# Kernel tuning notes

Hardware: AMD Instinct MI355X
Metric: run time of the kernel (lower is better)

## Reference

```python
import jax, jax.numpy as jnp
import numpy as np

B, T, D, H = 1024, 64, 256, 256  # batch, time steps, input_size, hidden_size


def setup_inputs() -> dict:
    key = jax.random.key(0)
    ks = jax.random.split(key, 5)
    s = 0.05
    return {
        "input_data": jax.random.normal(ks[0], (B, T, D), jnp.float32),
        # nn.Linear(2H+T, 1)
        "W_attn": jax.random.normal(ks[1], (1, 2 * H + T), jnp.float32) * s,
        "b_attn": jnp.zeros((1,), jnp.float32),
        # nn.LSTM(input_size=D, hidden_size=H, num_layers=1); gate order i,f,g,o
        "W_ih": jax.random.normal(ks[2], (4 * H, D), jnp.float32) * s,
        "W_hh": jax.random.normal(ks[3], (4 * H, H), jnp.float32) * s,
        "b_ih": jnp.zeros((4 * H,), jnp.float32),
        "b_hh": jnp.zeros((4 * H,), jnp.float32),
    }


def _encoder(input_data, W_attn, b_attn, W_ih, W_hh, b_ih, b_hh):
    Bv, Tv, Dv = input_data.shape
    Hv = W_hh.shape[1]
    # attn_linear applied to concat([h, c, x_series]) decomposes exactly into
    # three dot products (same math, no giant concat materialized each step).
    w_h = W_attn[0, :Hv]            # (H,)  weight on hidden part
    w_c = W_attn[0, Hv:2 * Hv]      # (H,)  weight on cell part
    w_x = W_attn[0, 2 * Hv:]        # (T,)  weight on per-feature time series
    # input_data.permute(0,2,1) @ w_x is constant across steps -> precompute.
    x_score = jnp.einsum('btd,t->bd', input_data, w_x) + b_attn[0]  # (B, D)

    xs = jnp.moveaxis(input_data, 1, 0)  # (T, B, D)

    def step(carry, x_t):
        h, c = carry                              # each (B, H)
        s_hc = h @ w_h + c @ w_c                  # (B,) same across features
        attn = jax.nn.softmax(s_hc[:, None] + x_score, axis=1)  # (B, D)
        w_in = attn * x_t                         # weighted input, (B, D)
        gates = w_in @ W_ih.T + h @ W_hh.T + b_ih + b_hh  # (B, 4H)
        i, f, g, o = jnp.split(gates, 4, axis=1)
        c_new = jax.nn.sigmoid(f) * c + jax.nn.sigmoid(i) * jnp.tanh(g)
        h_new = jax.nn.sigmoid(o) * jnp.tanh(c_new)
        return (h_new, c_new), (w_in, h_new)

    h0 = jnp.zeros((Bv, Hv), input_data.dtype)
    c0 = jnp.zeros((Bv, Hv), input_data.dtype)
    _, (ws, hs) = jax.lax.scan(step, (h0, c0), xs)
    input_weighted = jnp.moveaxis(ws, 0, 1)  # (B, T, D)
    input_encoded = jnp.moveaxis(hs, 0, 1)   # (B, T, H)
    return input_weighted, input_encoded


def reference(input_data, W_attn, b_attn, W_ih, W_hh, b_ih, b_hh):
    return _encoder(input_data, W_attn, b_attn, W_ih, W_hh, b_ih, b_hh)
```

## Files before the change

### kernel.cpp

```cpp
#include <hip/hip_runtime.h>
#include <hip/hip_bf16.h>
#include <stdint.h>

#define B_ 1024
#define T_ 64
#define D_ 256
#define H_ 256
#define G_ 1024

typedef float f32x4 __attribute__((ext_vector_type(4)));
typedef __bf16 bf16x8 __attribute__((ext_vector_type(8)));
typedef unsigned int u32x4 __attribute__((ext_vector_type(4)));

#if __has_builtin(__builtin_amdgcn_rcpf)
#define RCP(x) __builtin_amdgcn_rcpf(x)
#else
#define RCP(x) (1.f / (x))
#endif

__device__ __forceinline__ float bf2f(unsigned int u) {
    unsigned int x = u << 16;
    return __builtin_bit_cast(float, x);
}
__device__ __forceinline__ unsigned short f2bf(float f) {
    __hip_bfloat16 h = __float2bfloat16(f);
    return __builtin_bit_cast(unsigned short, h);
}

__global__ void prep_w_kernel(const float* __restrict__ Wih, const float* __restrict__ Whh,
                              const float* __restrict__ bih, const float* __restrict__ bhh,
                              unsigned short* __restrict__ wih_bf, unsigned short* __restrict__ whh_bf,
                              float* __restrict__ bias) {
    int i = blockIdx.x * 256 + threadIdx.x;
    wih_bf[i] = f2bf(Wih[i]);
    whh_bf[i] = f2bf(Whh[i]);
    if (i < G_) bias[i] = bih[i] + bhh[i];
}

__global__ void prep_attn_kernel(const float* __restrict__ x, const float* __restrict__ Wattn,
                                 float* __restrict__ attn) {
    __shared__ float wx[T_];
    __shared__ float red[256];
    int b = blockIdx.x, d = threadIdx.x;
    if (d < T_) wx[d] = Wattn[2 * H_ + d];
    __syncthreads();
    const float* xb = x + (size_t)b * T_ * D_ + d;
    float s = 0.f;
    #pragma unroll
    for (int t = 0; t < T_; ++t) s += xb[t * D_] * wx[t];
    red[d] = s;
    __syncthreads();
    for (int o = 128; o > 0; o >>= 1) {
        if (d < o) red[d] = fmaxf(red[d], red[d + o]);
        __syncthreads();
    }
    float m = red[0];
    __syncthreads();
    float e = __expf(s - m);
    red[d] = e;
    __syncthreads();
    for (int o = 128; o > 0; o >>= 1) {
        if (d < o) red[d] += red[d + o];
        __syncthreads();
    }
    attn[b * D_ + d] = e * (1.f / red[0]);
}

__global__ void winw_kernel(const float* __restrict__ x, const float* __restrict__ attn,
                            float* __restrict__ w_out, unsigned short* __restrict__ win_bf) {
    int i4 = blockIdx.x * 256 + threadIdx.x;
    int e  = i4 * 4;
    int d  = e & 255;
    int bt = e >> 8;
    int b  = bt >> 6, t = bt & 63;
    f32x4 xv = *(const f32x4*)(x + e);
    f32x4 av = *(const f32x4*)(attn + b * D_ + d);
    f32x4 w  = xv * av;
    *(f32x4*)(w_out + e) = w;
    ushort4 u;
    u.x = f2bf(w[0]); u.y = f2bf(w[1]); u.z = f2bf(w[2]); u.w = f2bf(w[3]);
    *(ushort4*)(win_bf + ((size_t)(t * B_ + b) * D_ + d)) = u;
}

__global__ __launch_bounds__(256, 2) void gemmx_kernel(const unsigned short* __restrict__ A,
                                                       const unsigned short* __restrict__ Bw,
                                                       unsigned short* __restrict__ pre) {
    int bx = blockIdx.x;
    int bn = bx & 7, bm = bx >> 3;
    int tid = threadIdx.x, lane = tid & 63, w = tid >> 6;
    int wr = w >> 1, wc = w & 1;
    int m0 = bm * 128 + wr * 64, n0 = bn * 128 + wc * 64;
    int lr = lane & 15, lk = (lane >> 4) * 8;

    const unsigned short* Ab[4];
    const unsigned short* Bb[4];
    #pragma unroll
    for (int i = 0; i < 4; ++i) {
        Ab[i] = A  + (size_t)(m0 + i * 16 + lr) * D_ + lk;
        Bb[i] = Bw + (size_t)(n0 + i * 16 + lr) * D_ + lk;
    }
    f32x4 acc[4][4] = {};
    #pragma unroll
    for (int kk = 0; kk < 8; ++kk) {
        bf16x8 a[4], bb[4];
        #pragma unroll
        for (int i = 0; i < 4; ++i) {
            a[i]  = *(const bf16x8*)(Ab[i] + kk * 32);
            bb[i] = *(const bf16x8*)(Bb[i] + kk * 32);
        }
        #pragma unroll
        for (int mi = 0; mi < 4; ++mi)
            #pragma unroll
            for (int ni = 0; ni < 4; ++ni)
                acc[mi][ni] = __builtin_amdgcn_mfma_f32_16x16x32_bf16(a[mi], bb[ni], acc[mi][ni], 0, 0, 0);
    }
    int orow = (lane >> 4) * 4;
    #pragma unroll
    for (int mi = 0; mi < 4; ++mi)
        #pragma unroll
        for (int ni = 0; ni < 4; ++ni)
            #pragma unroll
            for (int q = 0; q < 4; ++q) {
                int m = m0 + mi * 16 + orow + q;
                int n = n0 + ni * 16 + lr;
                pre[(size_t)m * G_ + n] = f2bf(acc[mi][ni][q]);
            }
}

__global__ __launch_bounds__(512)
__attribute__((amdgpu_waves_per_eu(2, 2)))
void seqs_kernel(const unsigned short* __restrict__ pre,
                 const unsigned short* __restrict__ Whh,
                 const float* __restrict__ bias,
                 float* __restrict__ enc_out) {
    extern __shared__ char smem[];
    unsigned short* W_frag = (unsigned short*)smem;
    unsigned short* h_frag = (unsigned short*)(smem + 131072);

    int tid = threadIdx.x, lane = tid & 63, w = tid >> 6;
    int lr = lane & 15, hi = lane >> 4;
    int r0 = blockIdx.x * 16;
    int j0 = w * 32;

    #pragma unroll
    for (int l = 0; l < 2; ++l) {
        int n = l * 256 + j0 + 16 + lr;
        const unsigned short* src = Whh + (size_t)n * 256 + hi * 8;
        #pragma unroll
        for (int c = 0; c < 8; ++c)
            *(u32x4*)&W_frag[(((w * 2 + l) * 8 + c) * 64 + lane) * 8] =
                *(const u32x4*)(src + c * 32);
    }
    for (int i = tid; i < 4096; i += 512) ((unsigned int*)h_frag)[i] = 0;

    bf16x8 Wreg[4][8];
    #pragma unroll
    for (int g = 0; g < 4; ++g)
        #pragma unroll
        for (int kk = 0; kk < 8; ++kk)
            Wreg[g][kk] = *(const bf16x8*)(Whh + (size_t)(g * 256 + j0 + lr) * 256 + kk * 32 + hi * 8);
    #pragma unroll
    for (int g = 0; g < 4; ++g)
        #pragma unroll
        for (int kk = 0; kk < 8; ++kk)
            asm volatile("" : "+a"(Wreg[g][kk]));

    bf16x8 Wreg2[2][8];
    #pragma unroll
    for (int s = 0; s < 2; ++s)
        #pragma unroll
        for (int kk = 0; kk < 8; ++kk)
            Wreg2[s][kk] = *(const bf16x8*)(Whh + (size_t)((s + 2) * 256 + j0 + 16 + lr) * 256 + kk * 32 + hi * 8);
    #pragma unroll
    for (int s = 0; s < 2; ++s)
        #pragma unroll
        for (int kk = 0; kk < 8; ++kk)
            asm volatile("" : "+v"(Wreg2[s][kk]));

    const unsigned short* ppair = pre + (size_t)(r0 + hi * 4) * G_ + j0 + (lr & 14);
    unsigned int sel = (lr & 1);
    float biasA[4], biasB[4];
    #pragma unroll
    for (int g = 0; g < 4; ++g) {
        biasA[g] = bias[g * 256 + j0 + lr];
        biasB[g] = bias[g * 256 + j0 + 16 + lr];
    }
    float cA[4] = {}, cB[4] = {};

    __syncthreads();

    #pragma unroll 1
    for (int t = 0; t < T_; ++t) {
        const unsigned short* Ps = ppair + (size_t)t * (1024u * 1024u);
        unsigned int pA[16];
        #pragma unroll
        for (int g = 0; g < 4; ++g)
            #pragma unroll
            for (int q = 0; q < 4; ++q)
                pA[g * 4 + q] = *(const unsigned int*)(Ps + (size_t)q * 1024 + g * 256);

        int p = t & 1;
        const unsigned short* hrd = h_frag + p * 4096;
        unsigned short*       hwr = h_frag + (p ^ 1) * 4096;

        f32x4 acc[4] = {};
        #pragma unroll
        for (int kk = 0; kk < 8; ++kk) {
            bf16x8 a = *(const bf16x8*)&hrd[(kk * 64 + lane) * 8];
            #pragma unroll
            for (int g = 0; g < 4; ++g)
                acc[g] = __builtin_amdgcn_mfma_f32_16x16x32_bf16(a, Wreg[g][kk], acc[g], 0, 0, 0);
        }

        unsigned int pB[16];
        #pragma unroll
        for (int g = 0; g < 4; ++g)
            #pragma unroll
            for (int q = 0; q < 4; ++q)
                pB[g * 4 + q] = *(const unsigned int*)(Ps + (size_t)q * 1024 + g * 256 + 16);

        #pragma unroll
        for (int q = 0; q < 4; ++q) {
            float gi = acc[0][q] + __builtin_bit_cast(float, sel ? (pA[0 * 4 + q] & 0xffff0000u) : (pA[0 * 4 + q] << 16)) + biasA[0];
            float gf = acc[1][q] + __builtin_bit_cast(float, sel ? (pA[1 * 4 + q] & 0xffff0000u) : (pA[1 * 4 + q] << 16)) + biasA[1];
            float gg = acc[2][q] + __builtin_bit_cast(float, sel ? (pA[2 * 4 + q] & 0xffff0000u) : (pA[2 * 4 + q] << 16)) + biasA[2];
            float go = acc[3][q] + __builtin_bit_cast(float, sel ? (pA[3 * 4 + q] & 0xffff0000u) : (pA[3 * 4 + q] << 16)) + biasA[3];
            float si = RCP(1.f + __expf(-gi));
            float sf = RCP(1.f + __expf(-gf));
            float so = RCP(1.f + __expf(-go));
            float tg = 1.f - 2.f * RCP(__expf(2.f * gg) + 1.f);
            float cn = sf * cA[q] + si * tg;
            cA[q] = cn;
            float tc = 1.f - 2.f * RCP(__expf(2.f * cn) + 1.f);
            float h  = so * tc;
            unsigned int hu = (unsigned int)f2bf(h);
            unsigned int ph = (unsigned int)__shfl_xor((int)hu, 1);
            if ((lr & 1) == 0) {
                unsigned int dw = hu | (ph << 16);
                *(unsigned int*)&hwr[w * 512 + (((lr >> 3) * 16) + hi * 4 + q) * 8 + (lr & 7)] = dw;
            }
            enc_out[((size_t)(r0 + hi * 4 + q) * T_ + t) * H_ + j0 + lr] = h;
        }

        f32x4 accB[4] = {};
        #pragma unroll
        for (int kk = 0; kk < 8; ++kk) {
            bf16x8 a  = *(const bf16x8*)&hrd[(kk * 64 + lane) * 8];
            bf16x8 b0 = *(const bf16x8*)&W_frag[(((w * 2 + 0) * 8 + kk) * 64 + lane) * 8];
            bf16x8 b1 = *(const bf16x8*)&W_frag[(((w * 2 + 1) * 8 + kk) * 64 + lane) * 8];
            accB[0] = __builtin_amdgcn_mfma_f32_16x16x32_bf16(a, b0, accB[0], 0, 0, 0);
            accB[1] = __builtin_amdgcn_mfma_f32_16x16x32_bf16(a, b1, accB[1], 0, 0, 0);
            accB[2] = __builtin_amdgcn_mfma_f32_16x16x32_bf16(a, Wreg2[0][kk], accB[2], 0, 0, 0);
            accB[3] = __builtin_amdgcn_mfma_f32_16x16x32_bf16(a, Wreg2[1][kk], accB[3], 0, 0, 0);
        }

        #pragma unroll
        for (int q = 0; q < 4; ++q) {
            float gi = accB[0][q] + __builtin_bit_cast(float, sel ? (pB[0 * 4 + q] & 0xffff0000u) : (pB[0 * 4 + q] << 16)) + biasB[0];
            float gf = accB[1][q] + __builtin_bit_cast(float, sel ? (pB[1 * 4 + q] & 0xffff0000u) : (pB[1 * 4 + q] << 16)) + biasB[1];
            float gg = accB[2][q] + __builtin_bit_cast(float, sel ? (pB[2 * 4 + q] & 0xffff0000u) : (pB[2 * 4 + q] << 16)) + biasB[2];
            float go = accB[3][q] + __builtin_bit_cast(float, sel ? (pB[3 * 4 + q] & 0xffff0000u) : (pB[3 * 4 + q] << 16)) + biasB[3];
            float si = RCP(1.f + __expf(-gi));
            float sf = RCP(1.f + __expf(-gf));
            float so = RCP(1.f + __expf(-go));
            float tg = 1.f - 2.f * RCP(__expf(2.f * gg) + 1.f);
            float cn = sf * cB[q] + si * tg;
            cB[q] = cn;
            float tc = 1.f - 2.f * RCP(__expf(2.f * cn) + 1.f);
            float h  = so * tc;
            unsigned int hu = (unsigned int)f2bf(h);
            unsigned int ph = (unsigned int)__shfl_xor((int)hu, 1);
            if ((lr & 1) == 0) {
                unsigned int dw = hu | (ph << 16);
                *(unsigned int*)&hwr[w * 512 + ((32 + (lr >> 3) * 16) + hi * 4 + q) * 8 + (lr & 7)] = dw;
            }
            enc_out[((size_t)(r0 + hi * 4 + q) * T_ + t) * H_ + j0 + 16 + lr] = h;
        }

        asm volatile("s_waitcnt lgkmcnt(0)" ::: "memory");
        __builtin_amdgcn_s_barrier();
        __builtin_amdgcn_sched_barrier(0);
    }
}

extern "C" void kernel_launch(void* const* d_in, const int* in_sizes, int n_in,
                              void* d_out, int out_size, void* d_ws, size_t ws_size,
                              hipStream_t stream) {
    const float* x     = (const float*)d_in[0];
    const float* Wattn = (const float*)d_in[1];
    const float* Wih   = (const float*)d_in[3];
    const float* Whh   = (const float*)d_in[4];
    const float* bih   = (const float*)d_in[5];
    const float* bhh   = (const float*)d_in[6];

    char* ws = (char*)d_ws;
    float*          attn   = (float*)(ws);
    unsigned short* win_bf = (unsigned short*)(ws + 1048576);
    unsigned short* wih_bf = (unsigned short*)(ws + 34603008);
    unsigned short* whh_bf = (unsigned short*)(ws + 35127296);
    float*          bias   = (float*)(ws + 35651584);
    unsigned short* pre    = (unsigned short*)(ws + 35659776);

    float* w_out   = (float*)d_out;
    float* enc_out = (float*)d_out + (size_t)B_ * T_ * D_;

    hipFuncSetAttribute((const void*)seqs_kernel,
                        hipFuncAttributeMaxDynamicSharedMemorySize, 147456);

    prep_w_kernel<<<dim3(1024), dim3(256), 0, stream>>>(Wih, Whh, bih, bhh, wih_bf, whh_bf, bias);
    prep_attn_kernel<<<dim3(1024), dim3(256), 0, stream>>>(x, Wattn, attn);
    winw_kernel<<<dim3(16384), dim3(256), 0, stream>>>(x, attn, w_out, win_bf);
    gemmx_kernel<<<dim3(4096), dim3(256), 0, stream>>>(win_bf, wih_bf, pre);
    seqs_kernel<<<dim3(64), dim3(512), 147456, stream>>>(pre, whh_bf, bias, enc_out);
}
```

Before: 477.2 us.

## Prefetch next-step gate preactivations and stream W_hh slices from global memory

Stops keeping two gate slices of W_hh resident in VGPRs for the whole recurrence. Those weights are now re-streamed from global memory in half-K chunks every timestep, with the next chunk loaded while the current MFMAs run. The precomputed input-gate values are prefetched one timestep ahead so their global-load latency overlaps the current step's compute. This frees registers and hides load latency, at the cost of extra global and L2 traffic per step and possible stalls if the streamed weight loads are not hidden.

```diff
diff --git a/kernel.cpp b/kernel.cpp
--- a/kernel.cpp
+++ b/kernel.cpp
@@ -165,17 +165,14 @@
         for (int kk = 0; kk < 8; ++kk)
             asm volatile("" : "+a"(Wreg[g][kk]));
 
-    bf16x8 Wreg2[2][8];
-    #pragma unroll
-    for (int s = 0; s < 2; ++s)
-        #pragma unroll
-        for (int kk = 0; kk < 8; ++kk)
-            Wreg2[s][kk] = *(const bf16x8*)(Whh + (size_t)((s + 2) * 256 + j0 + 16 + lr) * 256 + kk * 32 + hi * 8);
-    #pragma unroll
-    for (int s = 0; s < 2; ++s)
-        #pragma unroll
-        for (int kk = 0; kk < 8; ++kk)
-            asm volatile("" : "+v"(Wreg2[s][kk]));
+    const unsigned short* Ws0 = Whh + (size_t)(2 * 256 + j0 + 16 + lr) * 256 + hi * 8;
+    const unsigned short* Ws1 = Whh + (size_t)(3 * 256 + j0 + 16 + lr) * 256 + hi * 8;
+    bf16x8 sbuf[2][4];
+    #pragma unroll
+    for (int k2 = 0; k2 < 4; ++k2) {
+        sbuf[0][k2] = *(const bf16x8*)(Ws0 + k2 * 32);
+        sbuf[1][k2] = *(const bf16x8*)(Ws1 + k2 * 32);
+    }
 
     const unsigned short* ppair = pre + (size_t)(r0 + hi * 4) * G_ + j0 + (lr & 14);
     unsigned int sel = (lr & 1);
@@ -187,17 +184,20 @@
     }
     float cA[4] = {}, cB[4] = {};
 
+    unsigned int pA[16], pB[16];
+    #pragma unroll
+    for (int g = 0; g < 4; ++g)
+        #pragma unroll
+        for (int q = 0; q < 4; ++q) {
+            pA[g * 4 + q] = *(const unsigned int*)(ppair + (size_t)q * 1024 + g * 256);
+            pB[g * 4 + q] = *(const unsigned int*)(ppair + (size_t)q * 1024 + g * 256 + 16);
+        }
+
     __syncthreads();
 
     #pragma unroll 1
     for (int t = 0; t < T_; ++t) {
-        const unsigned short* Ps = ppair + (size_t)t * (1024u * 1024u);
-        unsigned int pA[16];
-        #pragma unroll
-        for (int g = 0; g < 4; ++g)
-            #pragma unroll
-            for (int q = 0; q < 4; ++q)
-                pA[g * 4 + q] = *(const unsigned int*)(Ps + (size_t)q * 1024 + g * 256);
+        const unsigned short* Pn = ppair + (size_t)(t < 63 ? t + 1 : 63) * (1024u * 1024u);
 
         int p = t & 1;
         const unsigned short* hrd = h_frag + p * 4096;
@@ -211,13 +211,6 @@
             for (int g = 0; g < 4; ++g)
                 acc[g] = __builtin_amdgcn_mfma_f32_16x16x32_bf16(a, Wreg[g][kk], acc[g], 0, 0, 0);
         }
-
-        unsigned int pB[16];
-        #pragma unroll
-        for (int g = 0; g < 4; ++g)
-            #pragma unroll
-            for (int q = 0; q < 4; ++q)
-                pB[g * 4 + q] = *(const unsigned int*)(Ps + (size_t)q * 1024 + g * 256 + 16);
 
         #pragma unroll
         for (int q = 0; q < 4; ++q) {
@@ -241,17 +234,47 @@
             }
             enc_out[((size_t)(r0 + hi * 4 + q) * T_ + t) * H_ + j0 + lr] = h;
         }
+        #pragma unroll
+        for (int g = 0; g < 4; ++g)
+            #pragma unroll
+            for (int q = 0; q < 4; ++q)
+                pA[g * 4 + q] = *(const unsigned int*)(Pn + (size_t)q * 1024 + g * 256);
 
         f32x4 accB[4] = {};
         #pragma unroll
-        for (int kk = 0; kk < 8; ++kk) {
+        for (int kk = 0; kk < 4; ++kk) {
             bf16x8 a  = *(const bf16x8*)&hrd[(kk * 64 + lane) * 8];
             bf16x8 b0 = *(const bf16x8*)&W_frag[(((w * 2 + 0) * 8 + kk) * 64 + lane) * 8];
             bf16x8 b1 = *(const bf16x8*)&W_frag[(((w * 2 + 1) * 8 + kk) * 64 + lane) * 8];
             accB[0] = __builtin_amdgcn_mfma_f32_16x16x32_bf16(a, b0, accB[0], 0, 0, 0);
             accB[1] = __builtin_amdgcn_mfma_f32_16x16x32_bf16(a, b1, accB[1], 0, 0, 0);
-            accB[2] = __builtin_amdgcn_mfma_f32_16x16x32_bf16(a, Wreg2[0][kk], accB[2], 0, 0, 0);
-            accB[3] = __builtin_amdgcn_mfma_f32_16x16x32_bf16(a, Wreg2[1][kk], accB[3], 0, 0, 0);
+            accB[2] = __builtin_amdgcn_mfma_f32_16x16x32_bf16(a, sbuf[0][kk], accB[2], 0, 0, 0);
+            accB[3] = __builtin_amdgcn_mfma_f32_16x16x32_bf16(a, sbuf[1][kk], accB[3], 0, 0, 0);
+        }
+        #pragma unroll
+        for (int k2 = 0; k2 < 4; ++k2) {
+            sbuf[0][k2] = *(const bf16x8*)(Ws0 + (k2 + 4) * 32);
+            sbuf[1][k2] = *(const bf16x8*)(Ws1 + (k2 + 4) * 32);
+        }
+        bf16x8 a47[4];
+        #pragma unroll
+        for (int kk = 4; kk < 8; ++kk) {
+            bf16x8 a  = *(const bf16x8*)&hrd[(kk * 64 + lane) * 8];
+            a47[kk - 4] = a;
+            bf16x8 b0 = *(const bf16x8*)&W_frag[(((w * 2 + 0) * 8 + kk) * 64 + lane) * 8];
+            bf16x8 b1 = *(const bf16x8*)&W_frag[(((w * 2 + 1) * 8 + kk) * 64 + lane) * 8];
+            accB[0] = __builtin_amdgcn_mfma_f32_16x16x32_bf16(a, b0, accB[0], 0, 0, 0);
+            accB[1] = __builtin_amdgcn_mfma_f32_16x16x32_bf16(a, b1, accB[1], 0, 0, 0);
+        }
+        #pragma unroll
+        for (int kk = 0; kk < 4; ++kk) {
+            accB[2] = __builtin_amdgcn_mfma_f32_16x16x32_bf16(a47[kk], sbuf[0][kk], accB[2], 0, 0, 0);
+            accB[3] = __builtin_amdgcn_mfma_f32_16x16x32_bf16(a47[kk], sbuf[1][kk], accB[3], 0, 0, 0);
+        }
+        #pragma unroll
+        for (int k2 = 0; k2 < 4; ++k2) {
+            sbuf[0][k2] = *(const bf16x8*)(Ws0 + k2 * 32);
+            sbuf[1][k2] = *(const bf16x8*)(Ws1 + k2 * 32);
         }
 
         #pragma unroll
@@ -276,6 +299,11 @@
             }
             enc_out[((size_t)(r0 + hi * 4 + q) * T_ + t) * H_ + j0 + 16 + lr] = h;
         }
+        #pragma unroll
+        for (int g = 0; g < 4; ++g)
+            #pragma unroll
+            for (int q = 0; q < 4; ++q)
+                pB[g * 4 + q] = *(const unsigned int*)(Pn + (size_t)q * 1024 + g * 256 + 16);
 
         asm volatile("s_waitcnt lgkmcnt(0)" ::: "memory");
         __builtin_amdgcn_s_barrier();
```

After: 664.8 us. 39.3% more time.
